# Optimization experiments

Measured on AMD Instinct MI355X. Metric: run time of the kernel, lower is better.

## Reference

```python
import jax, jax.numpy as jnp
import numpy as np

N_NODES = 100000
N_EDGES = 1600000
D = 128


def sage_conv(x, src, dst, W_l, W_r, b):
    # mean aggregation of source-node features at destination nodes
    msgs = x[src]  # [E, D] gather
    agg = jax.ops.segment_sum(msgs, dst, num_segments=N_NODES)  # [N, D]
    deg = jax.ops.segment_sum(jnp.ones((src.shape[0],), x.dtype), dst,
                              num_segments=N_NODES)
    agg = agg / jnp.maximum(deg, 1.0)[:, None]
    # PyG SAGEConv: lin_l(agg) + lin_r(x) (bias lives in lin_l)
    return agg @ W_l + x @ W_r + b


def setup_inputs() -> dict:
    key = jax.random.key(0)
    ks = jax.random.split(key, 8)
    s = 1.0 / np.sqrt(D)
    x = jax.random.normal(ks[0], (N_NODES, D), dtype=jnp.float32)
    edge_index = jax.random.randint(ks[1], (2, N_EDGES), 0, N_NODES, dtype=jnp.int64)
    W_l1 = jax.random.normal(ks[2], (D, D), dtype=jnp.float32) * s
    W_r1 = jax.random.normal(ks[3], (D, D), dtype=jnp.float32) * s
    b1 = jnp.zeros((D,), dtype=jnp.float32)
    W_l2 = jax.random.normal(ks[4], (D, D), dtype=jnp.float32) * s
    W_r2 = jax.random.normal(ks[5], (D, D), dtype=jnp.float32) * s
    b2 = jnp.zeros((D,), dtype=jnp.float32)
    return {"x": x, "edge_index": edge_index, "W_l1": W_l1, "W_r1": W_r1,
            "b1": b1, "W_l2": W_l2, "W_r2": W_r2, "b2": b2}


def reference(x, edge_index, W_l1, W_r1, b1, W_l2, W_r2, b2):
    src, dst = edge_index[0], edge_index[1]
    h = jax.nn.relu(sage_conv(x, src, dst, W_l1, W_r1, b1))
    h = jax.nn.relu(sage_conv(h, src, dst, W_l2, W_r2, b2))
    return h
```

## Files before the change

### kernel.cpp

```cpp
#include <hip/hip_runtime.h>
#include <hip/hip_bf16.h>
#include <stdint.h>

#define D 128
#define BCAP 18432
#define CPAD 32
#define HCAP 9216
typedef unsigned short u16;
typedef unsigned int u32;
typedef __attribute__((ext_vector_type(8))) short bf16x8;
typedef __attribute__((ext_vector_type(4))) float f32x4;
typedef __attribute__((ext_vector_type(2))) float f32x2;
typedef __attribute__((ext_vector_type(2))) unsigned int u32x2;

__device__ inline u16 f_to_bf16(float f) {
    u32 u = __builtin_bit_cast(u32, f);
    u += 0x7FFFu + ((u >> 16) & 1u);
    return (u16)(u >> 16);
}
__device__ inline u32 pack_bf16(float a, float b) {
    return (u32)f_to_bf16(a) | ((u32)f_to_bf16(b) << 16);
}

__global__ void zero_ints(int* __restrict__ p, int n) {
    int i = blockIdx.x * blockDim.x + threadIdx.x;
    if (i < n) p[i] = 0;
}

__global__ __launch_bounds__(256) void prep_fused(
    const int* __restrict__ src, const int* __restrict__ dst, int E, int nbuck, int binB,
    u32* __restrict__ pairs, int* __restrict__ bcur,
    const float* __restrict__ x, u16* __restrict__ xb, int nf4, int convB,
    const float* __restrict__ Wl1, const float* __restrict__ Wr1,
    const float* __restrict__ Wl2, const float* __restrict__ Wr2,
    u16* __restrict__ WT1, u16* __restrict__ WT2) {
    __shared__ int hist[128], gb[128], loc[128];
    int tid = threadIdx.x;
    int bid = blockIdx.x;
    if (bid < binB) {
        if (tid < 128) { hist[tid] = 0; loc[tid] = 0; }
        __syncthreads();
        int base = bid * 4096;
        int d[16], b[16];
        #pragma unroll
        for (int i = 0; i < 16; ++i) {
            int e = base + i * 256 + tid;
            d[i] = (e < E) ? dst[e] : -1;
            b[i] = (d[i] >= 0) ? (d[i] >> 10) : -1;
            if (b[i] >= 0) atomicAdd(&hist[b[i]], 1);
        }
        __syncthreads();
        if (tid < nbuck && hist[tid] > 0) gb[tid] = atomicAdd(&bcur[tid * CPAD], hist[tid]);
        __syncthreads();
        #pragma unroll
        for (int i = 0; i < 16; ++i) {
            if (b[i] >= 0) {
                int e = base + i * 256 + tid;
                int s = src[e];
                int r = atomicAdd(&loc[b[i]], 1);
                int pos = gb[b[i]] + r;
                if (pos < BCAP)
                    pairs[(size_t)b[i] * BCAP + pos] = ((u32)s << 10) | ((u32)d[i] & 1023u);
            }
        }
    } else if (bid < binB + convB) {
        int idx = (bid - binB) * 256 + tid;
        int stride = convB * 256;
        const float4* xf = (const float4*)x;
        uint2* xo = (uint2*)xb;
        for (int i = idx; i < nf4; i += stride) {
            float4 v = xf[i];
            xo[i] = make_uint2(pack_bf16(v.x, v.y), pack_bf16(v.z, v.w));
        }
    } else {
        int id = (bid - binB - convB) * 256 + tid;
        if (id < 2 * 128 * 256) {
            int which = id >> 15;
            int rem = id & 32767;
            int n = rem >> 8;
            int k = rem & 255;
            const float* Wl = which ? Wl2 : Wl1;
            const float* Wr = which ? Wr2 : Wr1;
            float v = (k < 128) ? Wl[k * 128 + n] : Wr[(k - 128) * 128 + n];
            u16* WT = which ? WT2 : WT1;
            WT[n * 256 + k] = f_to_bf16(v);
        }
    }
}

__global__ __launch_bounds__(1024) void build_csr(
    const u32* __restrict__ pairs, const int* __restrict__ bcur, int N,
    int* __restrict__ cnt, int* __restrict__ seg_start, int* __restrict__ gtotal,
    int* __restrict__ csr_src) {
    __shared__ int cnt_l[1024];
    __shared__ int off_l[1024];
    __shared__ int sblk[1024];
    __shared__ u32 stage[HCAP];
    __shared__ int gbase_s;
    int tid = threadIdx.x;
    int bk = blockIdx.x;
    int n0 = bk << 10;
    int nN = min(1024, N - n0);
    cnt_l[tid] = 0;
    __syncthreads();
    int m = min(bcur[bk * CPAD], BCAP);
    const u32* P = pairs + (size_t)bk * BCAP;
    for (int i = tid; i < m; i += 1024) {
        atomicAdd(&cnt_l[P[i] & 1023u], 1);
    }
    __syncthreads();
    int c = cnt_l[tid];
    sblk[tid] = c;
    for (int off = 1; off < 1024; off <<= 1) {
        __syncthreads();
        int u = (tid >= off) ? sblk[tid - off] : 0;
        __syncthreads();
        sblk[tid] += u;
    }
    int excl = sblk[tid] - c;
    off_l[tid] = excl;
    if (tid == 1023) gbase_s = atomicAdd(gtotal, sblk[1023]);
    __syncthreads();
    int gbase = gbase_s;
    if (tid < nN) {
        cnt[n0 + tid] = c;
        seg_start[n0 + tid] = gbase + excl;
    }
    int total = sblk[1023];
    int hstart1 = off_l[512];
    __syncthreads();
    #pragma unroll
    for (int half = 0; half < 2; ++half) {
        int hstart = half ? hstart1 : 0;
        int hcount = half ? (total - hstart1) : hstart1;
        if (hcount > HCAP) hcount = HCAP;
        if (tid < 512) cnt_l[tid] = 0;
        __syncthreads();
        for (int i = tid; i < m; i += 1024) {
            u32 e = P[i];
            int dl = (int)(e & 1023u);
            if ((dl >> 9) == half) {
                int r = atomicAdd(&cnt_l[dl & 511], 1);
                int idx = off_l[dl] - hstart + r;
                if (idx < HCAP) stage[idx] = e >> 10;
            }
        }
        __syncthreads();
        for (int j = tid; j < hcount; j += 1024)
            csr_src[gbase + hstart + j] = (int)stage[j];
        __syncthreads();
    }
}

__global__ __launch_bounds__(256) void aggregate_bf16(
    const u16* __restrict__ xb, const int* __restrict__ csr_src,
    const int* __restrict__ seg_start, const int* __restrict__ cnt,
    int N, u16* __restrict__ agg) {
    int wave = threadIdx.x >> 6;
    int lane = threadIdx.x & 63;
    int n = blockIdx.x * (blockDim.x >> 6) + wave;
    if (n >= N) return;
    int s0 = seg_start[n];
    int deg = cnt[n];
    int sub = lane & 15;
    int eoff = lane >> 4;

    f32x2 acc2[4];
    #pragma unroll
    for (int i = 0; i < 4; ++i) acc2[i] = (f32x2){0.f, 0.f};

    for (int c0 = 0; c0 < deg; c0 += 64) {
        int chunkN = min(deg - c0, 64);
        int myidx = (lane < chunkN) ? csr_src[s0 + c0 + lane] : 0;
        for (int e0 = 0; e0 < chunkN; e0 += 16) {
            uint4 v[4];
            #pragma unroll
            for (int j = 0; j < 4; ++j) {
                int ej = e0 + j * 4 + eoff;
                if (e0 + j * 4 < chunkN) {
                    int s = __shfl(myidx, ej & 63);
                    if (ej < chunkN)
                        v[j] = ((const uint4*)(xb + (size_t)s * 128))[sub];
                }
            }
            #pragma unroll
            for (int j = 0; j < 4; ++j) {
                int ej = e0 + j * 4 + eoff;
                if (ej < chunkN) {
                    u32 w;
                    w = v[j].x; acc2[0] += __builtin_bit_cast(f32x2, (u32x2){w << 16, w & 0xFFFF0000u});
                    w = v[j].y; acc2[1] += __builtin_bit_cast(f32x2, (u32x2){w << 16, w & 0xFFFF0000u});
                    w = v[j].z; acc2[2] += __builtin_bit_cast(f32x2, (u32x2){w << 16, w & 0xFFFF0000u});
                    w = v[j].w; acc2[3] += __builtin_bit_cast(f32x2, (u32x2){w << 16, w & 0xFFFF0000u});
                }
            }
        }
    }

    float a[8];
    #pragma unroll
    for (int i = 0; i < 4; ++i) { a[2 * i] = acc2[i].x; a[2 * i + 1] = acc2[i].y; }
    #pragma unroll
    for (int i = 0; i < 8; ++i) {
        a[i] += __shfl_xor(a[i], 16);
        a[i] += __shfl_xor(a[i], 32);
    }

    if (eoff == 0) {
        float inv = 1.0f / fmaxf((float)deg, 1.0f);
        uint4 o;
        o.x = pack_bf16(a[0] * inv, a[1] * inv);
        o.y = pack_bf16(a[2] * inv, a[3] * inv);
        o.z = pack_bf16(a[4] * inv, a[5] * inv);
        o.w = pack_bf16(a[6] * inv, a[7] * inv);
        ((uint4*)(agg + (size_t)n * 128))[sub] = o;
    }
}

template<int OUT_BF16>
__global__ __launch_bounds__(256) void sage_gemm(
    const u16* __restrict__ Aa, const u16* __restrict__ Ax,
    const u16* __restrict__ WT, const float* __restrict__ bias,
    void* __restrict__ out, int N) {
    __shared__ u16 Bl[128 * 256];
    int tid = threadIdx.x;

    {
        const uint4* Wg = (const uint4*)WT;
        uint4* Bl4 = (uint4*)Bl;
        #pragma unroll
        for (int i = 0; i < 16; ++i) {
            int cid = tid + 256 * i;
            int n = cid >> 5;
            int kc = cid & 31;
            Bl4[(n << 5) | (kc ^ (n & 15))] = Wg[cid];
        }
    }
    __syncthreads();

    int wavein = tid >> 6;
    int lane = tid & 63;
    int col = lane & 15;
    int chunk = lane >> 4;
    int wid = blockIdx.x * 4 + wavein;

    size_t m0 = (size_t)wid * 32 + col;
    size_t m1 = m0 + 16;
    size_t m0c = (m0 < (size_t)N) ? m0 : (size_t)(N - 1);
    size_t m1c = (m1 < (size_t)N) ? m1 : (size_t)(N - 1);

    const bf16x8* a0p = (const bf16x8*)(Aa + m0c * 128 + chunk * 8);
    const bf16x8* a1p = (const bf16x8*)(Aa + m1c * 128 + chunk * 8);
    const bf16x8* x0p = (const bf16x8*)(Ax + m0c * 128 + chunk * 8);
    const bf16x8* x1p = (const bf16x8*)(Ax + m1c * 128 + chunk * 8);

    f32x4 acc0[8], acc1[8];
    #pragma unroll
    for (int t = 0; t < 8; ++t) {
        acc0[t] = (f32x4){0.f, 0.f, 0.f, 0.f};
        acc1[t] = (f32x4){0.f, 0.f, 0.f, 0.f};
    }

    #pragma unroll
    for (int s = 0; s < 4; ++s) {
        bf16x8 a0 = a0p[s * 4];
        bf16x8 a1 = a1p[s * 4];
        int kc = s * 4 + chunk;
        #pragma unroll
        for (int t = 0; t < 8; ++t) {
            const bf16x8* bp = (const bf16x8*)(Bl + (((16 * t + col) << 8) | ((kc ^ col) << 3)));
            bf16x8 b = *bp;
            acc0[t] = __builtin_amdgcn_mfma_f32_16x16x32_bf16(a0, b, acc0[t], 0, 0, 0);
            acc1[t] = __builtin_amdgcn_mfma_f32_16x16x32_bf16(a1, b, acc1[t], 0, 0, 0);
        }
    }
    #pragma unroll
    for (int s = 0; s < 4; ++s) {
        bf16x8 a0 = x0p[s * 4];
        bf16x8 a1 = x1p[s * 4];
        int kc = 16 + s * 4 + chunk;
        #pragma unroll
        for (int t = 0; t < 8; ++t) {
            const bf16x8* bp = (const bf16x8*)(Bl + (((16 * t + col) << 8) | ((kc ^ col) << 3)));
            bf16x8 b = *bp;
            acc0[t] = __builtin_amdgcn_mfma_f32_16x16x32_bf16(a0, b, acc0[t], 0, 0, 0);
            acc1[t] = __builtin_amdgcn_mfma_f32_16x16x32_bf16(a1, b, acc1[t], 0, 0, 0);
        }
    }

    #pragma unroll
    for (int mt = 0; mt < 2; ++mt) {
        size_t row0 = (size_t)wid * 32 + mt * 16 + chunk * 4;
        #pragma unroll
        for (int t = 0; t < 8; ++t) {
            int n = 16 * t + col;
            float bv = bias[n];
            f32x4 a = mt ? acc1[t] : acc0[t];
            #pragma unroll
            for (int r = 0; r < 4; ++r) {
                size_t row = row0 + r;
                if (row < (size_t)N) {
                    float v = fmaxf(a[r] + bv, 0.f);
                    if (OUT_BF16) ((u16*)out)[row * 128 + n] = f_to_bf16(v);
                    else          ((float*)out)[row * 128 + n] = v;
                }
            }
        }
    }
}

extern "C" void kernel_launch(void* const* d_in, const int* in_sizes, int n_in,
                              void* d_out, int out_size, void* d_ws, size_t ws_size,
                              hipStream_t stream) {
    const float* x   = (const float*)d_in[0];
    const int*   ei  = (const int*)d_in[1];
    const float* Wl1 = (const float*)d_in[2];
    const float* Wr1 = (const float*)d_in[3];
    const float* b1  = (const float*)d_in[4];
    const float* Wl2 = (const float*)d_in[5];
    const float* Wr2 = (const float*)d_in[6];
    const float* b2  = (const float*)d_in[7];
    float* out       = (float*)d_out;

    int N = in_sizes[0] / D;
    int E = in_sizes[1] / 2;
    const int* src = ei;
    const int* dst = ei + E;
    int nbuck = (N + 1023) >> 10;

    char* ws = (char*)d_ws;
    int* cnt       = (int*)ws;  ws += (size_t)N * 4;
    int* seg_start = (int*)ws;  ws += (size_t)N * 4;
    int* bcur      = (int*)ws;  ws += 128 * CPAD * 4;
    int* gtotal    = (int*)ws;  ws += 4 * 4;
    ws = (char*)(((uintptr_t)ws + 255) & ~(uintptr_t)255);
    int* csr_src   = (int*)ws;  ws += (size_t)E * 4;
    ws = (char*)(((uintptr_t)ws + 255) & ~(uintptr_t)255);
    u16* WT1       = (u16*)ws;  ws += (size_t)128 * 256 * 2;
    u16* WT2       = (u16*)ws;  ws += (size_t)128 * 256 * 2;
    ws = (char*)(((uintptr_t)ws + 255) & ~(uintptr_t)255);
    u16* aggb      = (u16*)ws;  ws += (size_t)N * 128 * 2;
    ws = (char*)(((uintptr_t)ws + 255) & ~(uintptr_t)255);
    u16* h1b       = (u16*)ws;  ws += (size_t)N * 128 * 2;
    u16* xb        = (u16*)d_out;
    u32* pairs     = (u32*)aggb;

    zero_ints<<<(128 * CPAD + 4 + 255) / 256, 256, 0, stream>>>(bcur, 128 * CPAD + 4);

    int binB  = (E + 4095) / 4096;
    int convB = 2048;
    int nf4   = N * (D / 4);
    prep_fused<<<binB + convB + 256, 256, 0, stream>>>(
        src, dst, E, nbuck, binB, pairs, bcur,
        x, xb, nf4, convB, Wl1, Wr1, Wl2, Wr2, WT1, WT2);

    build_csr<<<nbuck, 1024, 0, stream>>>(pairs, bcur, N, cnt, seg_start, gtotal, csr_src);

    int aggBlocks = (N + 3) / 4;
    int gemmBlocks = (N + 127) / 128;

    aggregate_bf16<<<aggBlocks, 256, 0, stream>>>(xb, csr_src, seg_start, cnt, N, aggb);
    sage_gemm<1><<<gemmBlocks, 256, 0, stream>>>(aggb, xb, WT1, b1, h1b, N);

    aggregate_bf16<<<aggBlocks, 256, 0, stream>>>(h1b, csr_src, seg_start, cnt, N, aggb);
    sage_gemm<0><<<gemmBlocks, 256, 0, stream>>>(aggb, h1b, WT2, b2, out, N);
}
```

Baseline: 322.2 us.

## Fuse neighbor aggregation with SAGE GEMM per 16-node wave tile

Merges the aggregate and GEMM kernels into one. Each wave aggregates 16 destination nodes into a swizzled LDS tile, then runs MFMA on that tile against weights read straight from global memory. This removes the bf16 agg buffer round trip and two launches per layer. In exchange, weights are no longer staged in LDS, and each wave handles 16 nodes sequentially, so there is less parallelism and latency hiding in the gather phase.

```diff
diff --git a/kernel.cpp b/kernel.cpp
--- a/kernel.cpp
+++ b/kernel.cpp
@@ -152,158 +152,117 @@
     }
 }
 
-__global__ __launch_bounds__(256) void aggregate_bf16(
+template<int OUT_BF16>
+__global__ __launch_bounds__(256) void sage_fused(
     const u16* __restrict__ xb, const int* __restrict__ csr_src,
     const int* __restrict__ seg_start, const int* __restrict__ cnt,
-    int N, u16* __restrict__ agg) {
-    int wave = threadIdx.x >> 6;
+    const u16* __restrict__ WT, const float* __restrict__ bias,
+    void* __restrict__ out, int N) {
+    __shared__ u16 ldsA[4][16 * 128];
+    int wv = threadIdx.x >> 6;
     int lane = threadIdx.x & 63;
-    int n = blockIdx.x * (blockDim.x >> 6) + wave;
-    if (n >= N) return;
-    int s0 = seg_start[n];
-    int deg = cnt[n];
     int sub = lane & 15;
     int eoff = lane >> 4;
-
-    f32x2 acc2[4];
-    #pragma unroll
-    for (int i = 0; i < 4; ++i) acc2[i] = (f32x2){0.f, 0.f};
-
-    for (int c0 = 0; c0 < deg; c0 += 64) {
-        int chunkN = min(deg - c0, 64);
-        int myidx = (lane < chunkN) ? csr_src[s0 + c0 + lane] : 0;
-        for (int e0 = 0; e0 < chunkN; e0 += 16) {
-            uint4 v[4];
-            #pragma unroll
-            for (int j = 0; j < 4; ++j) {
-                int ej = e0 + j * 4 + eoff;
-                if (e0 + j * 4 < chunkN) {
-                    int s = __shfl(myidx, ej & 63);
-                    if (ej < chunkN)
-                        v[j] = ((const uint4*)(xb + (size_t)s * 128))[sub];
+    int nb = blockIdx.x * 64 + wv * 16;
+    u16* wl = ldsA[wv];
+
+    for (int nl = 0; nl < 16; ++nl) {
+        int n = nb + nl;
+        if (n >= N) break;
+        int s0 = seg_start[n];
+        int deg = cnt[n];
+        f32x2 acc2[4];
+        #pragma unroll
+        for (int i = 0; i < 4; ++i) acc2[i] = (f32x2){0.f, 0.f};
+        for (int c0 = 0; c0 < deg; c0 += 64) {
+            int chunkN = min(deg - c0, 64);
+            int myidx = (lane < chunkN) ? csr_src[s0 + c0 + lane] : 0;
+            for (int e0 = 0; e0 < chunkN; e0 += 16) {
+                uint4 v[4];
+                #pragma unroll
+                for (int j = 0; j < 4; ++j) {
+                    int ej = e0 + j * 4 + eoff;
+                    if (e0 + j * 4 < chunkN) {
+                        int s = __shfl(myidx, ej & 63);
+                        if (ej < chunkN)
+                            v[j] = ((const uint4*)(xb + (size_t)s * 128))[sub];
+                    }
+                }
+                #pragma unroll
+                for (int j = 0; j < 4; ++j) {
+                    int ej = e0 + j * 4 + eoff;
+                    if (ej < chunkN) {
+                        u32 w;
+                        w = v[j].x; acc2[0] += __builtin_bit_cast(f32x2, (u32x2){w << 16, w & 0xFFFF0000u});
+                        w = v[j].y; acc2[1] += __builtin_bit_cast(f32x2, (u32x2){w << 16, w & 0xFFFF0000u});
+                        w = v[j].z; acc2[2] += __builtin_bit_cast(f32x2, (u32x2){w << 16, w & 0xFFFF0000u});
+                        w = v[j].w; acc2[3] += __builtin_bit_cast(f32x2, (u32x2){w << 16, w & 0xFFFF0000u});
+                    }
                 }
             }
-            #pragma unroll
-            for (int j = 0; j < 4; ++j) {
-                int ej = e0 + j * 4 + eoff;
-                if (ej < chunkN) {
-                    u32 w;
-                    w = v[j].x; acc2[0] += __builtin_bit_cast(f32x2, (u32x2){w << 16, w & 0xFFFF0000u});
-                    w = v[j].y; acc2[1] += __builtin_bit_cast(f32x2, (u32x2){w << 16, w & 0xFFFF0000u});
-                    w = v[j].z; acc2[2] += __builtin_bit_cast(f32x2, (u32x2){w << 16, w & 0xFFFF0000u});
-                    w = v[j].w; acc2[3] += __builtin_bit_cast(f32x2, (u32x2){w << 16, w & 0xFFFF0000u});
-                }
-            }
-        }
-    }
-
-    float a[8];
-    #pragma unroll
-    for (int i = 0; i < 4; ++i) { a[2 * i] = acc2[i].x; a[2 * i + 1] = acc2[i].y; }
-    #pragma unroll
-    for (int i = 0; i < 8; ++i) {
-        a[i] += __shfl_xor(a[i], 16);
-        a[i] += __shfl_xor(a[i], 32);
-    }
-
-    if (eoff == 0) {
-        float inv = 1.0f / fmaxf((float)deg, 1.0f);
-        uint4 o;
-        o.x = pack_bf16(a[0] * inv, a[1] * inv);
-        o.y = pack_bf16(a[2] * inv, a[3] * inv);
-        o.z = pack_bf16(a[4] * inv, a[5] * inv);
-        o.w = pack_bf16(a[6] * inv, a[7] * inv);
-        ((uint4*)(agg + (size_t)n * 128))[sub] = o;
-    }
-}
-
-template<int OUT_BF16>
-__global__ __launch_bounds__(256) void sage_gemm(
-    const u16* __restrict__ Aa, const u16* __restrict__ Ax,
-    const u16* __restrict__ WT, const float* __restrict__ bias,
-    void* __restrict__ out, int N) {
-    __shared__ u16 Bl[128 * 256];
-    int tid = threadIdx.x;
-
-    {
-        const uint4* Wg = (const uint4*)WT;
-        uint4* Bl4 = (uint4*)Bl;
-        #pragma unroll
-        for (int i = 0; i < 16; ++i) {
-            int cid = tid + 256 * i;
-            int n = cid >> 5;
-            int kc = cid & 31;
-            Bl4[(n << 5) | (kc ^ (n & 15))] = Wg[cid];
-        }
-    }
-    __syncthreads();
-
-    int wavein = tid >> 6;
-    int lane = tid & 63;
-    int col = lane & 15;
-    int chunk = lane >> 4;
-    int wid = blockIdx.x * 4 + wavein;
-
-    size_t m0 = (size_t)wid * 32 + col;
-    size_t m1 = m0 + 16;
+        }
+        float a[8];
+        #pragma unroll
+        for (int i = 0; i < 4; ++i) { a[2 * i] = acc2[i].x; a[2 * i + 1] = acc2[i].y; }
+        #pragma unroll
+        for (int i = 0; i < 8; ++i) {
+            a[i] += __shfl_xor(a[i], 16);
+            a[i] += __shfl_xor(a[i], 32);
+        }
+        if (eoff == 0) {
+            float inv = 1.0f / fmaxf((float)deg, 1.0f);
+            uint4 o;
+            o.x = pack_bf16(a[0] * inv, a[1] * inv);
+            o.y = pack_bf16(a[2] * inv, a[3] * inv);
+            o.z = pack_bf16(a[4] * inv, a[5] * inv);
+            o.w = pack_bf16(a[6] * inv, a[7] * inv);
+            *(uint4*)&wl[nl * 128 + ((sub ^ nl) * 8)] = o;
+        }
+    }
+
+    int col = sub;
+    int chunk = eoff;
+    size_t m0 = (size_t)nb + col;
     size_t m0c = (m0 < (size_t)N) ? m0 : (size_t)(N - 1);
-    size_t m1c = (m1 < (size_t)N) ? m1 : (size_t)(N - 1);
-
-    const bf16x8* a0p = (const bf16x8*)(Aa + m0c * 128 + chunk * 8);
-    const bf16x8* a1p = (const bf16x8*)(Aa + m1c * 128 + chunk * 8);
-    const bf16x8* x0p = (const bf16x8*)(Ax + m0c * 128 + chunk * 8);
-    const bf16x8* x1p = (const bf16x8*)(Ax + m1c * 128 + chunk * 8);
-
-    f32x4 acc0[8], acc1[8];
-    #pragma unroll
-    for (int t = 0; t < 8; ++t) {
-        acc0[t] = (f32x4){0.f, 0.f, 0.f, 0.f};
-        acc1[t] = (f32x4){0.f, 0.f, 0.f, 0.f};
-    }
+    const bf16x8* x0p = (const bf16x8*)(xb + m0c * 128 + chunk * 8);
+
+    f32x4 acc[8];
+    #pragma unroll
+    for (int t = 0; t < 8; ++t) acc[t] = (f32x4){0.f, 0.f, 0.f, 0.f};
 
     #pragma unroll
     for (int s = 0; s < 4; ++s) {
-        bf16x8 a0 = a0p[s * 4];
-        bf16x8 a1 = a1p[s * 4];
         int kc = s * 4 + chunk;
+        bf16x8 a0 = *(const bf16x8*)&wl[col * 128 + ((kc ^ col) * 8)];
         #pragma unroll
         for (int t = 0; t < 8; ++t) {
-            const bf16x8* bp = (const bf16x8*)(Bl + (((16 * t + col) << 8) | ((kc ^ col) << 3)));
-            bf16x8 b = *bp;
-            acc0[t] = __builtin_amdgcn_mfma_f32_16x16x32_bf16(a0, b, acc0[t], 0, 0, 0);
-            acc1[t] = __builtin_amdgcn_mfma_f32_16x16x32_bf16(a1, b, acc1[t], 0, 0, 0);
+            bf16x8 b = *(const bf16x8*)(WT + (16 * t + col) * 256 + kc * 8);
+            acc[t] = __builtin_amdgcn_mfma_f32_16x16x32_bf16(a0, b, acc[t], 0, 0, 0);
         }
     }
     #pragma unroll
     for (int s = 0; s < 4; ++s) {
         bf16x8 a0 = x0p[s * 4];
-        bf16x8 a1 = x1p[s * 4];
         int kc = 16 + s * 4 + chunk;
         #pragma unroll
         for (int t = 0; t < 8; ++t) {
-            const bf16x8* bp = (const bf16x8*)(Bl + (((16 * t + col) << 8) | ((kc ^ col) << 3)));
-            bf16x8 b = *bp;
-            acc0[t] = __builtin_amdgcn_mfma_f32_16x16x32_bf16(a0, b, acc0[t], 0, 0, 0);
-            acc1[t] = __builtin_amdgcn_mfma_f32_16x16x32_bf16(a1, b, acc1[t], 0, 0, 0);
-        }
-    }
-
-    #pragma unroll
-    for (int mt = 0; mt < 2; ++mt) {
-        size_t row0 = (size_t)wid * 32 + mt * 16 + chunk * 4;
-        #pragma unroll
-        for (int t = 0; t < 8; ++t) {
-            int n = 16 * t + col;
-            float bv = bias[n];
-            f32x4 a = mt ? acc1[t] : acc0[t];
-            #pragma unroll
-            for (int r = 0; r < 4; ++r) {
-                size_t row = row0 + r;
-                if (row < (size_t)N) {
-                    float v = fmaxf(a[r] + bv, 0.f);
-                    if (OUT_BF16) ((u16*)out)[row * 128 + n] = f_to_bf16(v);
-                    else          ((float*)out)[row * 128 + n] = v;
-                }
+            bf16x8 b = *(const bf16x8*)(WT + (16 * t + col) * 256 + kc * 8);
+            acc[t] = __builtin_amdgcn_mfma_f32_16x16x32_bf16(a0, b, acc[t], 0, 0, 0);
+        }
+    }
+
+    size_t row0 = (size_t)nb + chunk * 4;
+    #pragma unroll
+    for (int t = 0; t < 8; ++t) {
+        int n = 16 * t + col;
+        float bv = bias[n];
+        #pragma unroll
+        for (int r = 0; r < 4; ++r) {
+            size_t row = row0 + r;
+            if (row < (size_t)N) {
+                float v = fmaxf(acc[t][r] + bv, 0.f);
+                if (OUT_BF16) ((u16*)out)[row * 128 + n] = f_to_bf16(v);
+                else          ((float*)out)[row * 128 + n] = v;
             }
         }
     }
@@ -339,11 +298,10 @@
     u16* WT1       = (u16*)ws;  ws += (size_t)128 * 256 * 2;
     u16* WT2       = (u16*)ws;  ws += (size_t)128 * 256 * 2;
     ws = (char*)(((uintptr_t)ws + 255) & ~(uintptr_t)255);
-    u16* aggb      = (u16*)ws;  ws += (size_t)N * 128 * 2;
+    u32* pairs     = (u32*)ws;  ws += (size_t)128 * BCAP * 4;
     ws = (char*)(((uintptr_t)ws + 255) & ~(uintptr_t)255);
     u16* h1b       = (u16*)ws;  ws += (size_t)N * 128 * 2;
     u16* xb        = (u16*)d_out;
-    u32* pairs     = (u32*)aggb;
 
     zero_ints<<<(128 * CPAD + 4 + 255) / 256, 256, 0, stream>>>(bcur, 128 * CPAD + 4);
 
@@ -356,12 +314,8 @@
 
     build_csr<<<nbuck, 1024, 0, stream>>>(pairs, bcur, N, cnt, seg_start, gtotal, csr_src);
 
-    int aggBlocks = (N + 3) / 4;
-    int gemmBlocks = (N + 127) / 128;
-
-    aggregate_bf16<<<aggBlocks, 256, 0, stream>>>(xb, csr_src, seg_start, cnt, N, aggb);
-    sage_gemm<1><<<gemmBlocks, 256, 0, stream>>>(aggb, xb, WT1, b1, h1b, N);
-
-    aggregate_bf16<<<aggBlocks, 256, 0, stream>>>(h1b, csr_src, seg_start, cnt, N, aggb);
-    sage_gemm<0><<<gemmBlocks, 256, 0, stream>>>(aggb, h1b, WT2, b2, out, N);
-}
+    int fusedBlocks = (N + 63) / 64;
+
+    sage_fused<1><<<fusedBlocks, 256, 0, stream>>>(xb, csr_src, seg_start, cnt, WT1, b1, h1b, N);
+    sage_fused<0><<<fusedBlocks, 256, 0, stream>>>(h1b, csr_src, seg_start, cnt, WT2, b2, out, N);
+}
```

Measured after the change: 541.0 us. 1.68x slower.
